# Kernel optimization log

Hardware: AMD Instinct MI355X
Metric: run time of the kernel (lower is better)

The kernel has to match this reference:

```python
import jax, jax.numpy as jnp
import numpy as np

ALPHA = 0.25
GAMMA = 2.0
EPS = 1e-8
COST_CLASS = 1.0
COST_BBOX = 1.0
COST_GIOU = 1.0


def segment_cw_to_t1t2(x):
    # x: [..., 2] = (center, width) -> (t1, t2)
    c, w = x[..., 0], x[..., 1]
    return jnp.stack([c - 0.5 * w, c + 0.5 * w], axis=-1)


def segment_iou(a, b):
    # a: [N, 2], b: [M, 2] -> pairwise IoU [N, M]
    lt = jnp.maximum(a[:, None, 0], b[None, :, 0])
    rb = jnp.minimum(a[:, None, 1], b[None, :, 1])
    inter = jnp.clip(rb - lt, 0.0)
    union = (a[:, 1] - a[:, 0])[:, None] + (b[:, 1] - b[:, 0])[None, :] - inter
    return inter / jnp.maximum(union, EPS)


def setup_inputs() -> dict:
    key = jax.random.key(0)
    k1, k2, k3, k4, k5, k6 = jax.random.split(key, 6)
    bs, Q, n_cls, M = 16, 2000, 80, 1024
    pred_logits = jax.random.normal(k1, (bs, Q, n_cls), dtype=jnp.float32)
    # boxes layout: [t1, t2, center, width] with t1<=t2 and width>0 (valid segments)
    p_t = jnp.sort(jax.random.uniform(k2, (bs, Q, 2), dtype=jnp.float32), axis=-1)
    p_cw = jax.random.uniform(k3, (bs, Q, 2), dtype=jnp.float32) * jnp.array([1.0, 0.5]) + jnp.array([0.0, 0.05])
    pred_boxes = jnp.concatenate([p_t, p_cw], axis=-1)
    t_t = jnp.sort(jax.random.uniform(k4, (M, 2), dtype=jnp.float32), axis=-1)
    t_cw = jax.random.uniform(k5, (M, 2), dtype=jnp.float32) * jnp.array([1.0, 0.5]) + jnp.array([0.0, 0.05])
    tgt_bbox = jnp.concatenate([t_t, t_cw], axis=-1)
    tgt_ids = jax.random.randint(k6, (M,), 0, n_cls, dtype=jnp.int64 if jax.config.jax_enable_x64 else jnp.int32)
    return {"pred_logits": pred_logits, "pred_boxes": pred_boxes,
            "tgt_ids": tgt_ids, "tgt_bbox": tgt_bbox}


def reference(pred_logits, pred_boxes, tgt_ids, tgt_bbox):
    bs, Q, _ = pred_logits.shape
    out_prob = jax.nn.softmax(pred_logits.reshape(bs * Q, -1), axis=-1)  # [bs*Q, n_cls]
    out_bbox = pred_boxes.reshape(bs * Q, 4)
    # focal-style classification cost
    neg_cost = (1.0 - ALPHA) * out_prob ** GAMMA * (-jnp.log1p(-out_prob + EPS))
    pos_cost = ALPHA * (1.0 - out_prob) ** GAMMA * (-jnp.log(out_prob + EPS))
    cost_class = pos_cost[:, tgt_ids] - neg_cost[:, tgt_ids]  # [bs*Q, M]
    # L1 box cost (cdist p=1)
    cost_bbox = jnp.sum(jnp.abs(out_bbox[:, None, :] - tgt_bbox[None, :, :]), axis=-1)
    # GIoU-style cost: average of IoU over (c,w)->t1t2 segments and raw t1t2 segments
    cost_giou = -(segment_iou(segment_cw_to_t1t2(out_bbox[:, 2:]), segment_cw_to_t1t2(tgt_bbox[:, 2:]))
                  + segment_iou(out_bbox[:, :2], tgt_bbox[:, :2])) / 2.0
    C = COST_BBOX * cost_bbox + COST_CLASS * cost_class + COST_GIOU * cost_giou
    return C.reshape(bs, Q, -1)
```

## Files before the change

### kernel.cpp

```cpp
#include <hip/hip_runtime.h>
#include <math.h>

#define ALPHA 0.25f
#define EPS 1e-8f

constexpr int NCLS = 80;
constexpr int Mn = 1024;
constexpr int RPB = 8;

__global__ __launch_bounds__(256) void matcher_kernel(
    const float* __restrict__ logits,
    const float* __restrict__ pboxes,
    const int*   __restrict__ tids,
    const float* __restrict__ tboxes,
    float* __restrict__ out)
{
    __shared__ float cls[RPB][NCLS];
    __shared__ float rowd[RPB][8];

    const int tid  = threadIdx.x;
    const int row0 = blockIdx.x * RPB;

    const int j0 = tid * 4;
    float4 tb[4]; int id[4]; float tt1[4], tt2[4], twr[4];
    #pragma unroll
    for (int k = 0; k < 4; ++k) {
        tb[k] = *(const float4*)(tboxes + (size_t)(j0 + k) * 4);
        id[k] = tids[j0 + k];
    }

    if (tid < 160) {
        ((float4*)&cls[0][0])[tid] =
            ((const float4*)(logits + (size_t)row0 * NCLS))[tid];
    }
    if (tid < RPB) {
        float4 pb = *(const float4*)(pboxes + (size_t)(row0 + tid) * 4);
        rowd[tid][0] = pb.x;
        rowd[tid][1] = pb.y;
        rowd[tid][2] = pb.z;
        rowd[tid][3] = pb.w;
        rowd[tid][4] = pb.z - 0.5f * pb.w;
        rowd[tid][5] = pb.z + 0.5f * pb.w;
        rowd[tid][6] = pb.y - pb.x;
        rowd[tid][7] = 0.0f;
    }
    #pragma unroll
    for (int k = 0; k < 4; ++k) {
        tt1[k] = tb[k].z - 0.5f * tb[k].w;
        tt2[k] = tb[k].z + 0.5f * tb[k].w;
        twr[k] = tb[k].y - tb[k].x;
    }
    __syncthreads();

    {
        const int r = tid >> 5;
        const int c = tid & 31;
        const int c2 = (c < 16) ? c + 64 : c;
        float l0 = cls[r][c];
        float l1 = cls[r][c + 32];
        float l2 = cls[r][c2];
        float e0 = __expf(l0);
        float e1 = __expf(l1);
        float e2 = (c < 16) ? __expf(l2) : 0.0f;
        float s = e0 + e1 + e2;
        #pragma unroll
        for (int off = 16; off; off >>= 1) s += __shfl_xor(s, off);
        float inv_s = __builtin_amdgcn_rcpf(s);
        float p0 = e0 * inv_s, p1 = e1 * inv_s, p2 = e2 * inv_s;

        float o0 = 1.0f - p0, o1 = 1.0f - p1, o2 = 1.0f - p2;
        float cc0 = ALPHA * o0 * o0 * (-__logf(p0 + EPS))
                  - (1.0f - ALPHA) * p0 * p0 * (-__logf(o0 + EPS));
        float cc1 = ALPHA * o1 * o1 * (-__logf(p1 + EPS))
                  - (1.0f - ALPHA) * p1 * p1 * (-__logf(o1 + EPS));
        float cc2 = ALPHA * o2 * o2 * (-__logf(p2 + EPS))
                  - (1.0f - ALPHA) * p2 * p2 * (-__logf(o2 + EPS));
        cls[r][c]      = cc0;
        cls[r][c + 32] = cc1;
        if (c < 16) cls[r][c + 64] = cc2;
    }
    __syncthreads();

    #pragma unroll
    for (int r = 0; r < RPB; ++r) {
        float4 ra = *(float4*)&rowd[r][0];
        float4 rb = *(float4*)&rowd[r][4];
        float4 res;
        #pragma unroll
        for (int k = 0; k < 4; ++k) {
            float db = fabsf(ra.x - tb[k].x) + fabsf(ra.y - tb[k].y)
                     + fabsf(ra.z - tb[k].z) + fabsf(ra.w - tb[k].w);
            float lt    = fmaxf(rb.x, tt1[k]);
            float rr    = fminf(rb.y, tt2[k]);
            float inter = fmaxf(rr - lt, 0.0f);
            float uni   = ra.w + tb[k].w - inter;
            float iou1  = inter * __builtin_amdgcn_rcpf(fmaxf(uni, EPS));
            float lt2    = fmaxf(ra.x, tb[k].x);
            float rr2    = fminf(ra.y, tb[k].y);
            float inter2 = fmaxf(rr2 - lt2, 0.0f);
            float uni2   = rb.z + twr[k] - inter2;
            float iou2   = inter2 * __builtin_amdgcn_rcpf(fmaxf(uni2, EPS));

            (&res.x)[k] = db + cls[r][id[k]] - 0.5f * (iou1 + iou2);
        }
        *(float4*)(out + (size_t)(row0 + r) * Mn + j0) = res;
    }
}

extern "C" void kernel_launch(void* const* d_in, const int* in_sizes, int n_in,
                              void* d_out, int out_size, void* d_ws, size_t ws_size,
                              hipStream_t stream) {
    const float* logits = (const float*)d_in[0];
    const float* pboxes = (const float*)d_in[1];
    const int*   tids   = (const int*)d_in[2];
    const float* tboxes = (const float*)d_in[3];
    float* out = (float*)d_out;

    const int total_rows = in_sizes[0] / NCLS;
    const int nblocks = total_rows / RPB;
    matcher_kernel<<<nblocks, 256, 0, stream>>>(logits, pboxes, tids, tboxes, out);
}
```

Baseline: 39.33 us.

## Pack target pairs into float2 math, merge IoU divisions, use nontemporal stores

Result: faster. 37.40 us (-4.9%).

```diff
diff --git a/kernel.cpp b/kernel.cpp
--- a/kernel.cpp
+++ b/kernel.cpp
@@ -3,6 +3,9 @@
 
 #define ALPHA 0.25f
 #define EPS 1e-8f
+
+typedef float f2 __attribute__((ext_vector_type(2)));
+typedef float f4v __attribute__((ext_vector_type(4)));
 
 constexpr int NCLS = 80;
 constexpr int Mn = 1024;
@@ -16,39 +19,29 @@
     float* __restrict__ out)
 {
     __shared__ float cls[RPB][NCLS];
-    __shared__ float rowd[RPB][8];
 
     const int tid  = threadIdx.x;
     const int row0 = blockIdx.x * RPB;
 
     const int j0 = tid * 4;
-    float4 tb[4]; int id[4]; float tt1[4], tt2[4], twr[4];
+    f2 tx[2], ty[2], tc[2], twh[2], twr[2];
+    int id[4];
     #pragma unroll
-    for (int k = 0; k < 4; ++k) {
-        tb[k] = *(const float4*)(tboxes + (size_t)(j0 + k) * 4);
-        id[k] = tids[j0 + k];
+    for (int p = 0; p < 2; ++p) {
+        float4 b0 = *(const float4*)(tboxes + (size_t)(j0 + 2 * p) * 4);
+        float4 b1 = *(const float4*)(tboxes + (size_t)(j0 + 2 * p + 1) * 4);
+        tx[p]  = f2{b0.x, b1.x};
+        ty[p]  = f2{b0.y, b1.y};
+        tc[p]  = f2{b0.z, b1.z};
+        twh[p] = f2{0.5f * b0.w, 0.5f * b1.w};
+        twr[p] = f2{b0.y - b0.x, b1.y - b1.x};
     }
+    #pragma unroll
+    for (int k = 0; k < 4; ++k) id[k] = tids[j0 + k];
 
     if (tid < 160) {
         ((float4*)&cls[0][0])[tid] =
             ((const float4*)(logits + (size_t)row0 * NCLS))[tid];
-    }
-    if (tid < RPB) {
-        float4 pb = *(const float4*)(pboxes + (size_t)(row0 + tid) * 4);
-        rowd[tid][0] = pb.x;
-        rowd[tid][1] = pb.y;
-        rowd[tid][2] = pb.z;
-        rowd[tid][3] = pb.w;
-        rowd[tid][4] = pb.z - 0.5f * pb.w;
-        rowd[tid][5] = pb.z + 0.5f * pb.w;
-        rowd[tid][6] = pb.y - pb.x;
-        rowd[tid][7] = 0.0f;
-    }
-    #pragma unroll
-    for (int k = 0; k < 4; ++k) {
-        tt1[k] = tb[k].z - 0.5f * tb[k].w;
-        tt2[k] = tb[k].z + 0.5f * tb[k].w;
-        twr[k] = tb[k].y - tb[k].x;
     }
     __syncthreads();
 
@@ -67,7 +60,6 @@
         for (int off = 16; off; off >>= 1) s += __shfl_xor(s, off);
         float inv_s = __builtin_amdgcn_rcpf(s);
         float p0 = e0 * inv_s, p1 = e1 * inv_s, p2 = e2 * inv_s;
-
         float o0 = 1.0f - p0, o1 = 1.0f - p1, o2 = 1.0f - p2;
         float cc0 = ALPHA * o0 * o0 * (-__logf(p0 + EPS))
                   - (1.0f - ALPHA) * p0 * p0 * (-__logf(o0 + EPS));
@@ -81,29 +73,49 @@
     }
     __syncthreads();
 
+    const f2 fzero = {0.0f, 0.0f};
+    const f2 feps  = {2.0f * EPS, 2.0f * EPS};
+
     #pragma unroll
     for (int r = 0; r < RPB; ++r) {
-        float4 ra = *(float4*)&rowd[r][0];
-        float4 rb = *(float4*)&rowd[r][4];
-        float4 res;
+        const float4 pb = *(const float4*)(pboxes + (size_t)(row0 + r) * 4);
+        const float rp0 = pb.x, rp1 = pb.y, rpc = pb.z, rpw = pb.w;
+        const float rpwh = 0.5f * pb.w;
+        const float rpwr = pb.y - pb.x;
+
+        const f2 ccv[2] = { f2{cls[r][id[0]], cls[r][id[1]]},
+                            f2{cls[r][id[2]], cls[r][id[3]]} };
+
+        f2 resp[2];
         #pragma unroll
-        for (int k = 0; k < 4; ++k) {
-            float db = fabsf(ra.x - tb[k].x) + fabsf(ra.y - tb[k].y)
-                     + fabsf(ra.z - tb[k].z) + fabsf(ra.w - tb[k].w);
-            float lt    = fmaxf(rb.x, tt1[k]);
-            float rr    = fminf(rb.y, tt2[k]);
-            float inter = fmaxf(rr - lt, 0.0f);
-            float uni   = ra.w + tb[k].w - inter;
-            float iou1  = inter * __builtin_amdgcn_rcpf(fmaxf(uni, EPS));
-            float lt2    = fmaxf(ra.x, tb[k].x);
-            float rr2    = fminf(ra.y, tb[k].y);
-            float inter2 = fmaxf(rr2 - lt2, 0.0f);
-            float uni2   = rb.z + twr[k] - inter2;
-            float iou2   = inter2 * __builtin_amdgcn_rcpf(fmaxf(uni2, EPS));
-
-            (&res.x)[k] = db + cls[r][id[k]] - 0.5f * (iou1 + iou2);
+        for (int p = 0; p < 2; ++p) {
+            f2 d1 = rp0 - tx[p];
+            f2 d2 = rp1 - ty[p];
+            f2 dc = rpc - tc[p];
+            f2 dw = rpwh - twh[p];
+            f2 ab = __builtin_elementwise_abs(d1) + __builtin_elementwise_abs(d2);
+            f2 db = ab + __builtin_elementwise_abs(dc)
+                       + 2.0f * __builtin_elementwise_abs(dw);
+            f2 a  = dc - dw;
+            f2 b  = dc + dw;
+            f2 P1 = rpw + 2.0f * twh[p];
+            f2 A1 = P1 - __builtin_elementwise_abs(a)
+                       - __builtin_elementwise_abs(b);
+            A1 = __builtin_elementwise_max(A1, fzero);
+            f2 D1 = __builtin_elementwise_max(2.0f * P1 - A1, feps);
+            f2 P2 = rpwr + twr[p];
+            f2 A2 = __builtin_elementwise_max(P2 - ab, fzero);
+            f2 D2 = __builtin_elementwise_max(2.0f * P2 - A2, feps);
+            f2 num = A1 * D2 + A2 * D1;
+            f2 den = D1 * D2;
+            f2 inv;
+            inv.x = __builtin_amdgcn_rcpf(den.x);
+            inv.y = __builtin_amdgcn_rcpf(den.y);
+            resp[p] = db + ccv[p] - 0.5f * (num * inv);
         }
-        *(float4*)(out + (size_t)(row0 + r) * Mn + j0) = res;
+        f4v res = {resp[0].x, resp[0].y, resp[1].x, resp[1].y};
+        __builtin_nontemporal_store(res,
+            (f4v*)(out + (size_t)(row0 + r) * Mn + j0));
     }
 }
 
```
